# Kernel optimization log

Hardware: AMD Instinct MI355X
Metric: run time of the kernel (lower is better)

Reference implementation:

```python
import jax, jax.numpy as jnp
import numpy as np

N_NODES = 100000
HID = 64
IN_DIM = 128


def setup_inputs() -> dict:
    key = jax.random.key(0)
    ks = jax.random.split(key, 12)
    x = jax.random.normal(ks[0], (N_NODES, IN_DIM), dtype=jnp.float32)
    edge_index = jax.random.randint(ks[1], (2, 1600000), 0, N_NODES, dtype=jnp.int64)
    batch = jnp.zeros((N_NODES,), dtype=jnp.int64)
    def glorot(k, shape):
        fan_in, fan_out = shape
        lim = (6.0 / (fan_in + fan_out)) ** 0.5
        return jax.random.uniform(k, shape, jnp.float32, -lim, lim)
    return {
        "x": x,
        "edge_index": edge_index,
        "batch": batch,
        "W1": glorot(ks[2], (IN_DIM, HID)), "b1": jnp.zeros((HID,), jnp.float32),
        "W2": glorot(ks[3], (HID, HID)),   "b2": jnp.zeros((HID,), jnp.float32),
        "W3": glorot(ks[4], (HID, HID)),   "b3": jnp.zeros((HID,), jnp.float32),
        "Wp1": glorot(ks[5], (HID, HID // 2)), "bp1": jnp.zeros((HID // 2,), jnp.float32),
        "Wp2": glorot(ks[6], (HID // 2, 1)),   "bp2": jnp.zeros((1,), jnp.float32),
    }


def _gcn_norm(edge_index, n_nodes):
    # Add self-loops, compute symmetric normalization deg^{-1/2}[src]*deg^{-1/2}[dst]
    loops = jnp.arange(n_nodes, dtype=edge_index.dtype)
    src = jnp.concatenate([edge_index[0], loops])
    dst = jnp.concatenate([edge_index[1], loops])
    deg = jax.ops.segment_sum(jnp.ones_like(dst, dtype=jnp.float32), dst,
                              num_segments=n_nodes)
    dinv = jnp.where(deg > 0, jax.lax.rsqrt(deg), 0.0)
    norm = dinv[src] * dinv[dst]  # [E + N]
    return src, dst, norm


def _gcn_layer(x, src, dst, norm, W, b, n_nodes):
    h = x @ W                       # [N, out]  dense transform first (PyG order)
    msg = h[src] * norm[:, None]    # gather + scale, [E+N, out]
    agg = jax.ops.segment_sum(msg, dst, num_segments=n_nodes)  # scatter-add
    return agg + b


def reference(x, edge_index, batch, W1, b1, W2, b2, W3, b3, Wp1, bp1, Wp2, bp2):
    n = x.shape[0]
    src, dst, norm = _gcn_norm(edge_index, n)
    # eval mode: dropout is identity
    h = jax.nn.relu(_gcn_layer(x, src, dst, norm, W1, b1, n))
    h = jax.nn.relu(_gcn_layer(h, src, dst, norm, W2, b2, n))
    h = jax.nn.relu(_gcn_layer(h, src, dst, norm, W3, b3, n))
    h = jax.nn.relu(h @ Wp1 + bp1)
    return h @ Wp2 + bp2  # [N, 1] node predictions
```

## Files before the change

### kernel.cpp

```cpp
#include <hip/hip_runtime.h>
#include <hip/hip_bf16.h>
#include <hip/hip_fp16.h>

#define NDIM_IN 128
#define HID 64

#define BINW 128
#define NB   782
#define NC   256
#define CAP  3072
#define CAPE 1024

typedef _Float16 f16x8 __attribute__((ext_vector_type(8)));
typedef float f32x4 __attribute__((ext_vector_type(4)));

#define MIX_LO(acc, hsrc) \
  asm("v_fma_mix_f32 %0, %1, %2, %0 op_sel:[0,0,0] op_sel_hi:[1,0,0]" \
      : "+v"(acc) : "v"(hsrc), "v"(one))
#define MIX_HI(acc, hsrc) \
  asm("v_fma_mix_f32 %0, %1, %2, %0 op_sel:[1,0,0] op_sel_hi:[1,0,0]" \
      : "+v"(acc) : "v"(hsrc), "v"(one))
#define ACC8(a, q) do { \
  MIX_LO(a[0], (q).x); MIX_HI(a[1], (q).x); \
  MIX_LO(a[2], (q).y); MIX_HI(a[3], (q).y); \
  MIX_LO(a[4], (q).z); MIX_HI(a[5], (q).z); \
  MIX_LO(a[6], (q).w); MIX_HI(a[7], (q).w); } while (0)

__global__ __launch_bounds__(1024) void hist_k(const int* __restrict__ dst,
                                               int* __restrict__ histT, int E) {
  __shared__ int h[NB];
  for (int i = threadIdx.x; i < NB; i += 1024) h[i] = 0;
  __syncthreads();
  int E4 = E >> 2;
  int chunk = (E4 + NC - 1) / NC;
  int beg = blockIdx.x * chunk;
  int end = min(E4, beg + chunk);
  const int4* __restrict__ d4 = (const int4*)dst;
  for (int i = beg + (int)threadIdx.x; i < end; i += 1024) {
    int4 d = d4[i];
    atomicAdd(&h[d.x >> 7], 1);
    atomicAdd(&h[d.y >> 7], 1);
    atomicAdd(&h[d.z >> 7], 1);
    atomicAdd(&h[d.w >> 7], 1);
  }
  __syncthreads();
  for (int i = threadIdx.x; i < NB; i += 1024)
    histT[i * NC + blockIdx.x] = h[i];
}

__global__ __launch_bounds__(256) void scan1(int* __restrict__ g,
                                             int* __restrict__ bs, int len) {
  __shared__ int s[256];
  int t = threadIdx.x;
  int i = blockIdx.x * 256 + t;
  int v = (i < len) ? g[i] : 0;
  s[t] = v;
  __syncthreads();
  for (int off = 1; off < 256; off <<= 1) {
    int x = (t >= off) ? s[t - off] : 0;
    __syncthreads();
    s[t] += x;
    __syncthreads();
  }
  if (i < len) g[i] = s[t] - v;
  if (t == 255) bs[blockIdx.x] = s[255];
}

__global__ __launch_bounds__(1024) void scatter_k(const int* __restrict__ src,
                                                  const int* __restrict__ dst,
                                                  const int* __restrict__ S,
                                                  const int* __restrict__ bs_raw,
                                                  int* __restrict__ bsum_out,
                                                  int* __restrict__ tmp, int E) {
  __shared__ int cur[NB];
  __shared__ int sc[1024];
  int t = threadIdx.x;
  int v = (t < NB) ? bs_raw[t] : 0;
  sc[t] = v;
  __syncthreads();
  for (int off = 1; off < 1024; off <<= 1) {
    int x = (t >= off) ? sc[t - off] : 0;
    __syncthreads();
    sc[t] += x;
    __syncthreads();
  }
  if (t < NB) {
    int ex = sc[t] - v;
    cur[t] = S[t * NC + blockIdx.x] + ex;
    if (blockIdx.x == 0) bsum_out[t] = ex;
  }
  __syncthreads();
  int E4 = E >> 2;
  int chunk = (E4 + NC - 1) / NC;
  int beg = blockIdx.x * chunk;
  int end = min(E4, beg + chunk);
  const int4* __restrict__ d4 = (const int4*)dst;
  const int4* __restrict__ s4 = (const int4*)src;
  for (int i = beg + (int)threadIdx.x; i < end; i += 1024) {
    int4 d = d4[i];
    int4 sv = s4[i];
    int p0 = atomicAdd(&cur[d.x >> 7], 1); tmp[p0] = (sv.x << 7) | (d.x & 127);
    int p1 = atomicAdd(&cur[d.y >> 7], 1); tmp[p1] = (sv.y << 7) | (d.y & 127);
    int p2 = atomicAdd(&cur[d.z >> 7], 1); tmp[p2] = (sv.z << 7) | (d.z & 127);
    int p3 = atomicAdd(&cur[d.w >> 7], 1); tmp[p3] = (sv.w << 7) | (d.w & 127);
  }
}

__global__ __launch_bounds__(256) void binsort_k(const int* __restrict__ tmp,
                                                 const int* __restrict__ bsum,
                                                 int* __restrict__ col,
                                                 int* __restrict__ rp,
                                                 float* __restrict__ dinv,
                                                 int n, int E) {
  int bin = blockIdx.x;
  int base = bsum[bin];
  int end = (bin == NB - 1) ? E : bsum[bin + 1];
  int m = end - base;
  __shared__ int cnt[BINW];
  __shared__ int offs[BINW];
  __shared__ int cur[BINW];
  __shared__ int buf[CAP];
  int t = threadIdx.x;
  if (t < BINW) cnt[t] = 0;
  __syncthreads();
  for (int i = t; i < m; i += 256) {
    int p = tmp[base + i];
    atomicAdd(&cnt[p & (BINW - 1)], 1);
  }
  __syncthreads();
  if (t < BINW) offs[t] = cnt[t];
  __syncthreads();
  for (int off = 1; off < BINW; off <<= 1) {
    int x = (t < BINW && t >= off) ? offs[t - off] : 0;
    __syncthreads();
    if (t < BINW) offs[t] += x;
    __syncthreads();
  }
  if (t < BINW) {
    int ex = offs[t] - cnt[t];
    cur[t] = ex;
    int v = bin * BINW + t;
    if (v < n) {
      rp[v] = base + ex;
      dinv[v] = rsqrtf((float)cnt[t] + 1.0f);
    }
  }
  if (bin == NB - 1 && t == 0) rp[n] = E;
  __syncthreads();
  for (int i = t; i < m; i += 256) {
    int p = tmp[base + i];
    int r = atomicAdd(&cur[p & (BINW - 1)], 1);
    if (r < CAP) buf[r] = p >> 7;
  }
  __syncthreads();
  int mm = min(m, CAP);
  for (int i = t; i < mm; i += 256) col[base + i] = buf[i];
}

template <int K, int FP16IN>
__global__ __launch_bounds__(256) void gemm_mfma(const void* __restrict__ Xv,
                                                 const float* __restrict__ W,
                                                 const float* __restrict__ dinv,
                                                 __half* __restrict__ T,
                                                 int n, int ntiles) {
  constexpr int NCH = K / 32;
  __shared__ float Ds[4][16 * 68];
  int wv = threadIdx.x >> 6;
  int lane = threadIdx.x & 63;
  int colx = lane & 15;
  int quad = lane >> 4;

  f16x8 bf[4][NCH];
#pragma unroll
  for (int t = 0; t < 4; t++)
#pragma unroll
    for (int c = 0; c < NCH; c++) {
      f16x8 b;
#pragma unroll
      for (int j = 0; j < 8; j++)
        b[j] = (_Float16)W[(32 * c + quad * 8 + j) * 64 + 16 * t + colx];
      bf[t][c] = b;
    }

  for (int tile = blockIdx.x * 4 + wv; tile < ntiles; tile += gridDim.x * 4) {
    int node0 = tile * 16;
    f32x4 acc[4] = {{0.f, 0.f, 0.f, 0.f}, {0.f, 0.f, 0.f, 0.f},
                    {0.f, 0.f, 0.f, 0.f}, {0.f, 0.f, 0.f, 0.f}};
    int arow = min(node0 + colx, n - 1);
#pragma unroll
    for (int c = 0; c < NCH; c++) {
      f16x8 a;
      if constexpr (FP16IN) {
        const _Float16* __restrict__ xr = (const _Float16*)Xv + (size_t)arow * K;
        a = *(const f16x8*)(xr + 32 * c + quad * 8);
      } else {
        const float* __restrict__ xr = (const float*)Xv + (size_t)arow * K;
        float4 x0 = *(const float4*)(xr + 32 * c + quad * 8);
        float4 x1 = *(const float4*)(xr + 32 * c + quad * 8 + 4);
        a[0] = (_Float16)x0.x; a[1] = (_Float16)x0.y;
        a[2] = (_Float16)x0.z; a[3] = (_Float16)x0.w;
        a[4] = (_Float16)x1.x; a[5] = (_Float16)x1.y;
        a[6] = (_Float16)x1.z; a[7] = (_Float16)x1.w;
      }
#pragma unroll
      for (int t = 0; t < 4; t++)
        acc[t] = __builtin_amdgcn_mfma_f32_16x16x32_f16(a, bf[t][c], acc[t], 0, 0, 0);
    }
    float dv[4];
#pragma unroll
    for (int r = 0; r < 4; r++) {
      int nd = min(node0 + quad * 4 + r, n - 1);
      dv[r] = dinv[nd];
    }
#pragma unroll
    for (int t = 0; t < 4; t++)
#pragma unroll
      for (int r = 0; r < 4; r++)
        Ds[wv][(quad * 4 + r) * 68 + 16 * t + colx] = acc[t][r] * dv[r];
    int nd = node0 + colx;
    const float* __restrict__ row = &Ds[wv][colx * 68 + quad * 16];
    float4 y0 = *(const float4*)(row + 0);
    float4 y1 = *(const float4*)(row + 4);
    float4 y2 = *(const float4*)(row + 8);
    float4 y3 = *(const float4*)(row + 12);
    f16x8 o0, o1;
    o0[0] = (_Float16)y0.x; o0[1] = (_Float16)y0.y;
    o0[2] = (_Float16)y0.z; o0[3] = (_Float16)y0.w;
    o0[4] = (_Float16)y1.x; o0[5] = (_Float16)y1.y;
    o0[6] = (_Float16)y1.z; o0[7] = (_Float16)y1.w;
    o1[0] = (_Float16)y2.x; o1[1] = (_Float16)y2.y;
    o1[2] = (_Float16)y2.z; o1[3] = (_Float16)y2.w;
    o1[4] = (_Float16)y3.x; o1[5] = (_Float16)y3.y;
    o1[6] = (_Float16)y3.z; o1[7] = (_Float16)y3.w;
    if (nd < n) {
      uint4* __restrict__ o = (uint4*)(T + (size_t)nd * 64 + quad * 16);
      o[0] = *(uint4*)&o0;
      o[1] = *(uint4*)&o1;
    }
  }
}

template <int MODE>
__global__ __launch_bounds__(256) void spmm_relu(const int* __restrict__ rp,
                                                 const int* __restrict__ col,
                                                 const __half* __restrict__ T,
                                                 const float* __restrict__ dinv,
                                                 const float* __restrict__ bias,
                                                 void* __restrict__ Hout, int n) {
  __shared__ int colS[CAPE];
  int v0 = blockIdx.x * 32;
  int ebeg = rp[v0];
  int eend = rp[min(v0 + 32, n)];
  int m = eend - ebeg;
  int mstage = min(m, CAPE);
  for (int i = threadIdx.x; i < mstage; i += 256) colS[i] = col[ebeg + i];
  __syncthreads();

  int lane = threadIdx.x & 63;
  int wv = threadIdx.x >> 6;
  int g = lane >> 3;
  int sub = lane & 7;
  int v = v0 + wv * 8 + g;
  bool valid = v < n;
  if (!valid) v = n - 1;
  const uint4* __restrict__ T8 = (const uint4*)T;
  int beg = rp[v];
  int end = rp[v + 1];
  int lim = min(end, ebeg + CAPE);

  float one = 1.0f;
  float a0[8], a1[8];
#pragma unroll
  for (int j = 0; j < 8; j++) { a0[j] = 0.f; a1[j] = 0.f; }
  {
    uint4 q0 = T8[(size_t)v * 8 + sub];
    ACC8(a0, q0);
  }
  int e = beg;
  for (; e + 4 <= lim; e += 4) {
    int s0 = colS[e - ebeg];
    int s1 = colS[e - ebeg + 1];
    int s2 = colS[e - ebeg + 2];
    int s3 = colS[e - ebeg + 3];
    uint4 q0 = T8[(size_t)s0 * 8 + sub];
    uint4 q1 = T8[(size_t)s1 * 8 + sub];
    uint4 q2 = T8[(size_t)s2 * 8 + sub];
    uint4 q3 = T8[(size_t)s3 * 8 + sub];
    ACC8(a0, q0);
    ACC8(a1, q1);
    ACC8(a0, q2);
    ACC8(a1, q3);
  }
  for (; e < lim; ++e) {
    int s0 = colS[e - ebeg];
    uint4 q0 = T8[(size_t)s0 * 8 + sub];
    ACC8(a0, q0);
  }
  for (; e < end; ++e) {
    int s0 = col[e];
    uint4 q0 = T8[(size_t)s0 * 8 + sub];
    ACC8(a0, q0);
  }
  float di = dinv[v];
  const float4* __restrict__ b4 = (const float4*)bias;
  float4 bA = b4[sub * 2], bB = b4[sub * 2 + 1];
  float4 rA, rB;
  rA.x = di * (a0[0] + a1[0]) + bA.x;
  rA.y = di * (a0[1] + a1[1]) + bA.y;
  rA.z = di * (a0[2] + a1[2]) + bA.z;
  rA.w = di * (a0[3] + a1[3]) + bA.w;
  rB.x = di * (a0[4] + a1[4]) + bB.x;
  rB.y = di * (a0[5] + a1[5]) + bB.y;
  rB.z = di * (a0[6] + a1[6]) + bB.z;
  rB.w = di * (a0[7] + a1[7]) + bB.w;
  rA.x = rA.x > 0.f ? rA.x : 0.f;  rA.y = rA.y > 0.f ? rA.y : 0.f;
  rA.z = rA.z > 0.f ? rA.z : 0.f;  rA.w = rA.w > 0.f ? rA.w : 0.f;
  rB.x = rB.x > 0.f ? rB.x : 0.f;  rB.y = rB.y > 0.f ? rB.y : 0.f;
  rB.z = rB.z > 0.f ? rB.z : 0.f;  rB.w = rB.w > 0.f ? rB.w : 0.f;
  if (valid) {
    if constexpr (MODE == 0) {
      f16x8 o;
      o[0] = (_Float16)rA.x; o[1] = (_Float16)rA.y;
      o[2] = (_Float16)rA.z; o[3] = (_Float16)rA.w;
      o[4] = (_Float16)rB.x; o[5] = (_Float16)rB.y;
      o[6] = (_Float16)rB.z; o[7] = (_Float16)rB.w;
      uint4* __restrict__ o4 = (uint4*)((__half*)Hout + (size_t)v * HID + sub * 8);
      *o4 = *(uint4*)&o;
    } else {
      float4* __restrict__ o = (float4*)((float*)Hout + (size_t)v * HID + sub * 8);
      o[0] = rA;
      o[1] = rB;
    }
  }
}

__global__ __launch_bounds__(256) void mlp_head(const float* __restrict__ H,
                                                const float* __restrict__ Wp1,
                                                const float* __restrict__ bp1,
                                                const float* __restrict__ Wp2,
                                                const float* __restrict__ bp2,
                                                float* __restrict__ out, int n) {
  __shared__ float W1t[32 * 64];
  __shared__ float w2s[32];
  __shared__ float b1s[32];
  for (int i = threadIdx.x; i < 64 * 32; i += 256) {
    int k = i >> 5, j = i & 31;
    W1t[j * 64 + k] = Wp1[i];
  }
  if (threadIdx.x < 32) {
    w2s[threadIdx.x] = Wp2[threadIdx.x];
    b1s[threadIdx.x] = bp1[threadIdx.x];
  }
  __syncthreads();
  int node = blockIdx.x * 256 + threadIdx.x;
  if (node >= n) return;
  float4 h[16];
  const float4* __restrict__ hr = (const float4*)(H + (size_t)node * 64);
#pragma unroll
  for (int j = 0; j < 16; j++) h[j] = hr[j];
  float o = bp2[0];
#pragma unroll
  for (int j = 0; j < 32; j++) {
    const float4* wr = (const float4*)(W1t + j * 64);
    float4 a4 = make_float4(0.f, 0.f, 0.f, 0.f);
#pragma unroll
    for (int k = 0; k < 16; k++) {
      float4 w = wr[k];
      a4.x += h[k].x * w.x;
      a4.y += h[k].y * w.y;
      a4.z += h[k].z * w.z;
      a4.w += h[k].w * w.w;
    }
    float a = a4.x + a4.y + a4.z + a4.w + b1s[j];
    a = a > 0.f ? a : 0.f;
    o += a * w2s[j];
  }
  out[node] = o;
}

extern "C" void kernel_launch(void* const* d_in, const int* in_sizes, int n_in,
                              void* d_out, int out_size, void* d_ws, size_t ws_size,
                              hipStream_t stream) {
  const float* x   = (const float*)d_in[0];
  const int* edge  = (const int*)d_in[1];
  const float* W1  = (const float*)d_in[3];
  const float* b1  = (const float*)d_in[4];
  const float* W2  = (const float*)d_in[5];
  const float* b2  = (const float*)d_in[6];
  const float* W3  = (const float*)d_in[7];
  const float* b3  = (const float*)d_in[8];
  const float* Wp1 = (const float*)d_in[9];
  const float* bp1 = (const float*)d_in[10];
  const float* Wp2 = (const float*)d_in[11];
  const float* bp2 = (const float*)d_in[12];
  float* out = (float*)d_out;

  const int n = in_sizes[0] / NDIM_IN;
  const int E = in_sizes[1] / 2;
  const int* src = edge;
  const int* dst = edge + E;

  char* ws = (char*)d_ws;
  size_t off = 0;
  auto carve = [&](size_t bytes) {
    char* p = ws + off;
    off = (off + bytes + 255) & ~(size_t)255;
    return p;
  };
  int*    histT = (int*)carve((size_t)NB * NC * 4);
  int*    bsraw = (int*)carve(1024 * 4);
  int*    bsum  = (int*)carve(1024 * 4);
  int*    tmp   = (int*)carve((size_t)E * 4);
  int*    col   = (int*)carve((size_t)E * 4);
  int*    rp    = (int*)carve(((size_t)n + 1) * 4);
  float*  dinv  = (float*)carve((size_t)n * 4);
  __half* bufT  = (__half*)carve((size_t)n * HID * 2);
  float*  bufA  = (float*)carve((size_t)n * HID * 4);
  __half* bufH  = (__half*)bufA;
  (void)ws_size; (void)n_in; (void)out_size;

  const int nbN = (n + 255) / 256;
  const int ntiles = (n + 15) >> 4;
  const int nbM = 782;
  const int scan_len = NB * NC;
  const int nbScan = (scan_len + 255) / 256;

  hist_k<<<NC, 1024, 0, stream>>>(dst, histT, E);
  scan1<<<nbScan, 256, 0, stream>>>(histT, bsraw, scan_len);
  scatter_k<<<NC, 1024, 0, stream>>>(src, dst, histT, bsraw, bsum, tmp, E);
  binsort_k<<<NB, 256, 0, stream>>>(tmp, bsum, col, rp, dinv, n, E);

  const int nbSp = (n + 31) / 32;

  gemm_mfma<128, 0><<<nbM, 256, 0, stream>>>(x, W1, dinv, bufT, n, ntiles);
  spmm_relu<0><<<nbSp, 256, 0, stream>>>(rp, col, bufT, dinv, b1, bufH, n);
  gemm_mfma<64, 1><<<nbM, 256, 0, stream>>>(bufH, W2, dinv, bufT, n, ntiles);
  spmm_relu<0><<<nbSp, 256, 0, stream>>>(rp, col, bufT, dinv, b2, bufH, n);
  gemm_mfma<64, 1><<<nbM, 256, 0, stream>>>(bufH, W3, dinv, bufT, n, ntiles);
  spmm_relu<1><<<nbSp, 256, 0, stream>>>(rp, col, bufT, dinv, b3, bufA, n);
  mlp_head<<<nbN, 256, 0, stream>>>(bufA, Wp1, bp1, Wp2, bp2, out, n);
}
```

Baseline: 183.0 us.

## Replace histogram scan with atomic bin offsets, unroll spmm, use fp16 final features

Removes the separate scan kernel by having each histogram block atomically reserve its offset within each bin. This also requires a memset of the bin counters. The spmm inner loop gains an 8-edge unrolled stage to keep more gathers in flight. The last GCN layer now writes fp16 instead of fp32, which halves the traffic into the MLP head. The costs are nondeterministic within-bin block ordering, extra register pressure, and slightly lower precision in the final layer.

After: 209.7 us. 14.5% more time.

```diff
diff --git a/kernel.cpp b/kernel.cpp
--- a/kernel.cpp
+++ b/kernel.cpp
@@ -27,7 +27,8 @@
   MIX_LO(a[6], (q).w); MIX_HI(a[7], (q).w); } while (0)
 
 __global__ __launch_bounds__(1024) void hist_k(const int* __restrict__ dst,
-                                               int* __restrict__ histT, int E) {
+                                               int* __restrict__ histT,
+                                               int* __restrict__ gofs, int E) {
   __shared__ int h[NB];
   for (int i = threadIdx.x; i < NB; i += 1024) h[i] = 0;
   __syncthreads();
@@ -44,38 +45,23 @@
     atomicAdd(&h[d.w >> 7], 1);
   }
   __syncthreads();
-  for (int i = threadIdx.x; i < NB; i += 1024)
-    histT[i * NC + blockIdx.x] = h[i];
-}
-
-__global__ __launch_bounds__(256) void scan1(int* __restrict__ g,
-                                             int* __restrict__ bs, int len) {
-  __shared__ int s[256];
-  int t = threadIdx.x;
-  int i = blockIdx.x * 256 + t;
-  int v = (i < len) ? g[i] : 0;
-  s[t] = v;
-  __syncthreads();
-  for (int off = 1; off < 256; off <<= 1) {
-    int x = (t >= off) ? s[t - off] : 0;
-    __syncthreads();
-    s[t] += x;
-    __syncthreads();
-  }
-  if (i < len) g[i] = s[t] - v;
-  if (t == 255) bs[blockIdx.x] = s[255];
+  for (int i = threadIdx.x; i < NB; i += 1024) {
+    int c = h[i];
+    int ofs = atomicAdd(&gofs[i], c);
+    histT[i * NC + blockIdx.x] = ofs;
+  }
 }
 
 __global__ __launch_bounds__(1024) void scatter_k(const int* __restrict__ src,
                                                   const int* __restrict__ dst,
                                                   const int* __restrict__ S,
-                                                  const int* __restrict__ bs_raw,
+                                                  const int* __restrict__ gofs,
                                                   int* __restrict__ bsum_out,
                                                   int* __restrict__ tmp, int E) {
   __shared__ int cur[NB];
   __shared__ int sc[1024];
   int t = threadIdx.x;
-  int v = (t < NB) ? bs_raw[t] : 0;
+  int v = (t < NB) ? gofs[t] : 0;
   sc[t] = v;
   __syncthreads();
   for (int off = 1; off < 1024; off <<= 1) {
@@ -240,13 +226,12 @@
   }
 }
 
-template <int MODE>
 __global__ __launch_bounds__(256) void spmm_relu(const int* __restrict__ rp,
                                                  const int* __restrict__ col,
                                                  const __half* __restrict__ T,
                                                  const float* __restrict__ dinv,
                                                  const float* __restrict__ bias,
-                                                 void* __restrict__ Hout, int n) {
+                                                 __half* __restrict__ Hout, int n) {
   __shared__ int colS[CAPE];
   int v0 = blockIdx.x * 32;
   int ebeg = rp[v0];
@@ -277,6 +262,32 @@
     ACC8(a0, q0);
   }
   int e = beg;
+  for (; e + 8 <= lim; e += 8) {
+    int s0 = colS[e - ebeg];
+    int s1 = colS[e - ebeg + 1];
+    int s2 = colS[e - ebeg + 2];
+    int s3 = colS[e - ebeg + 3];
+    int s4 = colS[e - ebeg + 4];
+    int s5 = colS[e - ebeg + 5];
+    int s6 = colS[e - ebeg + 6];
+    int s7 = colS[e - ebeg + 7];
+    uint4 q0 = T8[(size_t)s0 * 8 + sub];
+    uint4 q1 = T8[(size_t)s1 * 8 + sub];
+    uint4 q2 = T8[(size_t)s2 * 8 + sub];
+    uint4 q3 = T8[(size_t)s3 * 8 + sub];
+    uint4 q4 = T8[(size_t)s4 * 8 + sub];
+    uint4 q5 = T8[(size_t)s5 * 8 + sub];
+    uint4 q6 = T8[(size_t)s6 * 8 + sub];
+    uint4 q7 = T8[(size_t)s7 * 8 + sub];
+    ACC8(a0, q0);
+    ACC8(a1, q1);
+    ACC8(a0, q2);
+    ACC8(a1, q3);
+    ACC8(a0, q4);
+    ACC8(a1, q5);
+    ACC8(a0, q6);
+    ACC8(a1, q7);
+  }
   for (; e + 4 <= lim; e += 4) {
     int s0 = colS[e - ebeg];
     int s1 = colS[e - ebeg + 1];
@@ -318,23 +329,17 @@
   rB.x = rB.x > 0.f ? rB.x : 0.f;  rB.y = rB.y > 0.f ? rB.y : 0.f;
   rB.z = rB.z > 0.f ? rB.z : 0.f;  rB.w = rB.w > 0.f ? rB.w : 0.f;
   if (valid) {
-    if constexpr (MODE == 0) {
-      f16x8 o;
-      o[0] = (_Float16)rA.x; o[1] = (_Float16)rA.y;
-      o[2] = (_Float16)rA.z; o[3] = (_Float16)rA.w;
-      o[4] = (_Float16)rB.x; o[5] = (_Float16)rB.y;
-      o[6] = (_Float16)rB.z; o[7] = (_Float16)rB.w;
-      uint4* __restrict__ o4 = (uint4*)((__half*)Hout + (size_t)v * HID + sub * 8);
-      *o4 = *(uint4*)&o;
-    } else {
-      float4* __restrict__ o = (float4*)((float*)Hout + (size_t)v * HID + sub * 8);
-      o[0] = rA;
-      o[1] = rB;
-    }
-  }
-}
-
-__global__ __launch_bounds__(256) void mlp_head(const float* __restrict__ H,
+    f16x8 o;
+    o[0] = (_Float16)rA.x; o[1] = (_Float16)rA.y;
+    o[2] = (_Float16)rA.z; o[3] = (_Float16)rA.w;
+    o[4] = (_Float16)rB.x; o[5] = (_Float16)rB.y;
+    o[6] = (_Float16)rB.z; o[7] = (_Float16)rB.w;
+    uint4* __restrict__ o4 = (uint4*)(Hout + (size_t)v * HID + sub * 8);
+    *o4 = *(uint4*)&o;
+  }
+}
+
+__global__ __launch_bounds__(256) void mlp_head(const __half* __restrict__ H,
                                                 const float* __restrict__ Wp1,
                                                 const float* __restrict__ bp1,
                                                 const float* __restrict__ Wp2,
@@ -355,9 +360,19 @@
   int node = blockIdx.x * 256 + threadIdx.x;
   if (node >= n) return;
   float4 h[16];
-  const float4* __restrict__ hr = (const float4*)(H + (size_t)node * 64);
-#pragma unroll
-  for (int j = 0; j < 16; j++) h[j] = hr[j];
+  const uint4* __restrict__ hr = (const uint4*)(H + (size_t)node * 64);
+#pragma unroll
+  for (int j = 0; j < 8; j++) {
+    uint4 q = hr[j];
+    const __half2* h2 = (const __half2*)&q;
+    float2 f0 = __half22float2(h2[0]);
+    float2 f1 = __half22float2(h2[1]);
+    float2 f2 = __half22float2(h2[2]);
+    float2 f3 = __half22float2(h2[3]);
+    h[2 * j].x = f0.x; h[2 * j].y = f0.y; h[2 * j].z = f1.x; h[2 * j].w = f1.y;
+    h[2 * j + 1].x = f2.x; h[2 * j + 1].y = f2.y;
+    h[2 * j + 1].z = f3.x; h[2 * j + 1].w = f3.y;
+  }
   float o = bp2[0];
 #pragma unroll
   for (int j = 0; j < 32; j++) {
@@ -408,35 +423,32 @@
     return p;
   };
   int*    histT = (int*)carve((size_t)NB * NC * 4);
-  int*    bsraw = (int*)carve(1024 * 4);
+  int*    gofs  = (int*)carve(1024 * 4);
   int*    bsum  = (int*)carve(1024 * 4);
   int*    tmp   = (int*)carve((size_t)E * 4);
   int*    col   = (int*)carve((size_t)E * 4);
   int*    rp    = (int*)carve(((size_t)n + 1) * 4);
   float*  dinv  = (float*)carve((size_t)n * 4);
   __half* bufT  = (__half*)carve((size_t)n * HID * 2);
-  float*  bufA  = (float*)carve((size_t)n * HID * 4);
-  __half* bufH  = (__half*)bufA;
+  __half* bufH  = (__half*)carve((size_t)n * HID * 2);
   (void)ws_size; (void)n_in; (void)out_size;
 
   const int nbN = (n + 255) / 256;
   const int ntiles = (n + 15) >> 4;
   const int nbM = 782;
-  const int scan_len = NB * NC;
-  const int nbScan = (scan_len + 255) / 256;
-
-  hist_k<<<NC, 1024, 0, stream>>>(dst, histT, E);
-  scan1<<<nbScan, 256, 0, stream>>>(histT, bsraw, scan_len);
-  scatter_k<<<NC, 1024, 0, stream>>>(src, dst, histT, bsraw, bsum, tmp, E);
+
+  hipMemsetAsync(gofs, 0, NB * 4, stream);
+  hist_k<<<NC, 1024, 0, stream>>>(dst, histT, gofs, E);
+  scatter_k<<<NC, 1024, 0, stream>>>(src, dst, histT, gofs, bsum, tmp, E);
   binsort_k<<<NB, 256, 0, stream>>>(tmp, bsum, col, rp, dinv, n, E);
 
   const int nbSp = (n + 31) / 32;
 
   gemm_mfma<128, 0><<<nbM, 256, 0, stream>>>(x, W1, dinv, bufT, n, ntiles);
-  spmm_relu<0><<<nbSp, 256, 0, stream>>>(rp, col, bufT, dinv, b1, bufH, n);
+  spmm_relu<<<nbSp, 256, 0, stream>>>(rp, col, bufT, dinv, b1, bufH, n);
   gemm_mfma<64, 1><<<nbM, 256, 0, stream>>>(bufH, W2, dinv, bufT, n, ntiles);
-  spmm_relu<0><<<nbSp, 256, 0, stream>>>(rp, col, bufT, dinv, b2, bufH, n);
+  spmm_relu<<<nbSp, 256, 0, stream>>>(rp, col, bufT, dinv, b2, bufH, n);
   gemm_mfma<64, 1><<<nbM, 256, 0, stream>>>(bufH, W3, dinv, bufT, n, ntiles);
-  spmm_relu<1><<<nbSp, 256, 0, stream>>>(rp, col, bufT, dinv, b3, bufA, n);
-  mlp_head<<<nbN, 256, 0, stream>>>(bufA, Wp1, bp1, Wp2, bp2, out, n);
-}
+  spmm_relu<<<nbSp, 256, 0, stream>>>(rp, col, bufT, dinv, b3, bufH, n);
+  mlp_head<<<nbN, 256, 0, stream>>>(bufH, Wp1, bp1, Wp2, bp2, out, n);
+}
```
